# Kernel tuning notes

Hardware: AMD Instinct MI355X
Metric: run time of the kernel (lower is better)

The kernel has to match this reference:

```python
import jax, jax.numpy as jnp
import numpy as np

EPS_BN = 1e-5     # torch BatchNorm1d default eps
EPS_NORM = 1e-12  # torch F.normalize default eps


def _l2norm(x):
    n = jnp.linalg.norm(x, axis=-1, keepdims=True)
    return x / jnp.maximum(n, EPS_NORM)


def setup_inputs() -> dict:
    key = jax.random.key(0)
    ks = jax.random.split(key, 12)
    B, D, H, Z, E, C = 8192, 2048, 2048, 256, 5, 100

    def rn(k, shape, scale=1.0):
        return jax.random.normal(k, shape, dtype=jnp.float32) * scale

    feats = rn(ks[0], (B, D))
    # head_pattern: MLP(D->H->Z) with BN(H), prototypes Linear(Z->E, no bias)
    pW1 = rn(ks[1], (D, H), 1.0 / np.sqrt(D))
    pb1 = jnp.zeros((H,), jnp.float32)
    pg = jnp.ones((H,), jnp.float32)
    pbt = jnp.zeros((H,), jnp.float32)
    pm = jnp.zeros((H,), jnp.float32)
    pv = jnp.ones((H,), jnp.float32)
    pW2 = rn(ks[2], (H, Z), 1.0 / np.sqrt(H))
    pb2 = jnp.zeros((Z,), jnp.float32)
    pProto = _l2norm(rn(ks[3], (E, Z)))  # normalize_prototypes()
    # head_class: E experts, each MLP(Z->H->Z) with BN(H), prototypes Linear(Z->C, no bias)
    cW1 = rn(ks[4], (E, Z, H), 1.0 / np.sqrt(Z))
    cb1 = jnp.zeros((E, H), jnp.float32)
    cg = jnp.ones((E, H), jnp.float32)
    cbt = jnp.zeros((E, H), jnp.float32)
    cm = jnp.zeros((E, H), jnp.float32)
    cv = jnp.ones((E, H), jnp.float32)
    cW2 = rn(ks[5], (E, H, Z), 1.0 / np.sqrt(H))
    cb2 = jnp.zeros((E, Z), jnp.float32)
    cProto = _l2norm(rn(ks[6], (E, C, Z)))
    return dict(feats=feats, pW1=pW1, pb1=pb1, pg=pg, pbt=pbt, pm=pm, pv=pv,
                pW2=pW2, pb2=pb2, pProto=pProto, cW1=cW1, cb1=cb1, cg=cg,
                cbt=cbt, cm=cm, cv=cv, cW2=cW2, cb2=cb2, cProto=cProto)


def reference(feats, pW1, pb1, pg, pbt, pm, pv, pW2, pb2, pProto,
              cW1, cb1, cg, cbt, cm, cv, cW2, cb2, cProto):
    E = cW1.shape[0]
    # --- head_pattern (expert 0 only) ---
    h = feats @ pW1 + pb1                                   # [B,H]
    h = (h - pm) * jax.lax.rsqrt(pv + EPS_BN) * pg + pbt    # BN (eval)
    h = jax.nn.relu(h)
    zp = _l2norm(h @ pW2 + pb2)                             # proj_feats_pattern [B,Z]
    logits_pattern = zp @ pProto.T                          # [B,E]
    # --- routing: argmax over pattern logits ---
    route = jnp.argmax(logits_pattern, axis=1)              # [B]
    onehot = jax.nn.one_hot(route, E, dtype=zp.dtype)       # [B,E]
    # --- all experts densely, then per-sample select (E=5 is small) ---
    h2 = jnp.einsum('bz,ezh->ebh', zp, cW1) + cb1[:, None, :]          # [E,B,H]
    h2 = (h2 - cm[:, None, :]) * jax.lax.rsqrt(cv[:, None, :] + EPS_BN) \
         * cg[:, None, :] + cbt[:, None, :]
    h2 = jax.nn.relu(h2)
    z2 = _l2norm(jnp.einsum('ebh,ehz->ebz', h2, cW2) + cb2[:, None, :])  # [E,B,Z]
    lc = jnp.einsum('ebz,ecz->ebc', z2, cProto)                          # [E,B,C]
    logits_class = jnp.einsum('be,ebc->bc', onehot, lc)                  # [B,C]
    proj_feats_class = jnp.einsum('be,ebz->bz', onehot, z2)              # [B,Z]
    return logits_pattern, zp, logits_class, proj_feats_class
```

## Files before the change

kernel.cpp:

```cpp
#include <hip/hip_runtime.h>
#include <math.h>

#define EPS_BN   1e-5f
#define EPS_NORM 1e-12f
#define GAP_TAU  1e-3f
#define RMAX     1024

constexpr int B_ = 8192, D_ = 2048, H_ = 2048, Z_ = 256, E_ = 5, C_ = 100;

typedef __attribute__((ext_vector_type(8))) short short8v;
typedef __attribute__((ext_vector_type(4))) float f32x4;
typedef __attribute__((ext_vector_type(8))) unsigned short ush8;
typedef __attribute__((ext_vector_type(4))) unsigned short ush4;

#define MFMA16(a,b,c) __builtin_amdgcn_mfma_f32_16x16x32_bf16(a,b,c,0,0,0)

#define GLD_LDS16(SRC, DST) \
  __builtin_amdgcn_global_load_lds((const __attribute__((address_space(1))) void*)(SRC), \
                                   (__attribute__((address_space(3))) void*)(DST), 16, 0, 0)

__device__ inline unsigned short f2bf(float x) {
    union { float f; unsigned u; } a; a.f = x;
    unsigned r = a.u + 0x7FFFu + ((a.u >> 16) & 1u);
    return (unsigned short)(r >> 16);
}
__device__ inline float bf2f(unsigned short u) {
    union { float f; unsigned v; } a; a.v = ((unsigned)u) << 16;
    return a.f;
}

__global__ void zero_counts(int* counts) {
    if (threadIdx.x < 8) counts[threadIdx.x] = 0;
}

__global__ __launch_bounds__(256)
void pack_rows(const float* __restrict__ in, unsigned short* __restrict__ out, int K)
{
    const size_t base = ((size_t)blockIdx.x * 256 + threadIdx.x) * 8;
    const size_t row = base / (size_t)K;
    const int col = (int)(base % (size_t)K);
    const float4 v0 = *(const float4*)&in[base];
    const float4 v1 = *(const float4*)&in[base + 4];
    float v[8] = {v0.x, v0.y, v0.z, v0.w, v1.x, v1.y, v1.z, v1.w};
    ush8 hv, lv;
#pragma unroll
    for (int j = 0; j < 8; ++j) {
        unsigned short hi = f2bf(v[j]);
        hv[j] = hi;
        lv[j] = f2bf(v[j] - bf2f(hi));
    }
    const size_t ob = ((size_t)row * (K >> 5) + (col >> 5)) * 64 + (col & 31);
    *(ush8*)&out[ob] = hv;
    *(ush8*)&out[ob + 32] = lv;
}

template<bool PACKED>
__global__ __launch_bounds__(256)
void tconv_kernel(const float* __restrict__ in, unsigned short* __restrict__ out,
                  int K, int N)
{
    __shared__ float tile[32][33];
    const int kt = blockIdx.x, nt = blockIdx.y;
    const size_t inB = (size_t)blockIdx.z * K * N;
    const int t = threadIdx.x;
    const int lr = t >> 5, lc = t & 31;
#pragma unroll
    for (int i = 0; i < 4; ++i) {
        const int k = kt * 32 + lr + i * 8;
        tile[lr + i * 8][lc] = in[inB + (size_t)k * N + nt * 32 + lc];
    }
    __syncthreads();
    const int n_loc = t >> 3, s = t & 7;
    const int n = nt * 32 + n_loc;
    if (PACKED) {
        const size_t ob = (size_t)blockIdx.z * N * K * 2 +
                          ((size_t)n * (K >> 5) + kt) * 64;
        ush4 hv, lv;
#pragma unroll
        for (int j = 0; j < 4; ++j) {
            const float v = tile[s * 4 + j][n_loc];
            unsigned short hi = f2bf(v);
            hv[j] = hi;
            lv[j] = f2bf(v - bf2f(hi));
        }
        *(ush4*)&out[ob + s * 4] = hv;
        *(ush4*)&out[ob + 32 + s * 4] = lv;
    } else {
        const size_t ob = (size_t)blockIdx.z * N * K + (size_t)n * K + kt * 32;
        ush4 hv;
#pragma unroll
        for (int j = 0; j < 4; ++j) hv[j] = f2bf(tile[s * 4 + j][n_loc]);
        *(ush4*)&out[ob + s * 4] = hv;
    }
}

template<int BM, int BN, int EPI>
__global__ __launch_bounds__(256)
void gemm_split3(const unsigned short* __restrict__ Apk,
                 const unsigned short* __restrict__ Bpk,
                 const float* __restrict__ bias,
                 const float* __restrict__ g, const float* __restrict__ bt,
                 const float* __restrict__ mean, const float* __restrict__ var,
                 void* __restrict__ outp, int K, int N)
{
    constexpr int WM = BM / 2, WN = BN / 2, FM = WM / 16, FN = WN / 16;
    constexpr int ROWS = BM + BN, TI = ROWS / 8, PW = TI / 4;
    __shared__ __align__(16) unsigned short lds[ROWS * 64];
    const int tid = threadIdx.x, waveId = tid >> 6, lane = tid & 63;
    const int aRowBase = blockIdx.y * BM, bColBase = blockIdx.x * BN;
    const int wRow = (waveId >> 1) * WM, wCol = (waveId & 1) * WN;
    const int Kg = K >> 5;
    const int sr = lane >> 3, ss = lane & 7;

    f32x4 acc[FM][FN] = {};

    for (int kg = 0; kg < Kg; ++kg) {
#pragma unroll
        for (int t = 0; t < PW; ++t) {
            const int q = waveId * PW + t;
            const int r = q * 8 + sr;
            const int c = ss ^ (r & 7);
            const unsigned short* src;
            if (r < BM) src = Apk + ((size_t)(aRowBase + r) * Kg + kg) * 64 + c * 8;
            else        src = Bpk + ((size_t)(bColBase + (r - BM)) * Kg + kg) * 64 + c * 8;
            GLD_LDS16(src, &lds[q * 512]);
        }
        __syncthreads();
        short8v a_hi[FM], a_lo[FM], b_hi[FN], b_lo[FN];
#pragma unroll
        for (int fm = 0; fm < FM; ++fm) {
            const int r = wRow + fm * 16 + (lane & 15);
            const int ch = lane >> 4;
            a_hi[fm] = *(const short8v*)&lds[r * 64 + ((ch) ^ (r & 7)) * 8];
            a_lo[fm] = *(const short8v*)&lds[r * 64 + ((ch + 4) ^ (r & 7)) * 8];
        }
#pragma unroll
        for (int fn = 0; fn < FN; ++fn) {
            const int r = BM + wCol + fn * 16 + (lane & 15);
            const int ch = lane >> 4;
            b_hi[fn] = *(const short8v*)&lds[r * 64 + ((ch) ^ (r & 7)) * 8];
            b_lo[fn] = *(const short8v*)&lds[r * 64 + ((ch + 4) ^ (r & 7)) * 8];
        }
#pragma unroll
        for (int fm = 0; fm < FM; ++fm)
#pragma unroll
            for (int fn = 0; fn < FN; ++fn) {
                acc[fm][fn] = MFMA16(a_hi[fm], b_hi[fn], acc[fm][fn]);
                acc[fm][fn] = MFMA16(a_hi[fm], b_lo[fn], acc[fm][fn]);
                acc[fm][fn] = MFMA16(a_lo[fm], b_hi[fn], acc[fm][fn]);
            }
        __syncthreads();
    }

#pragma unroll
    for (int fn = 0; fn < FN; ++fn) {
        const int col = bColBase + wCol + fn * 16 + (lane & 15);
        const float bcol = bias[col];
        float scl = 0.f, sft = 0.f;
        if constexpr (EPI == 0) {
            scl = rsqrtf(var[col] + EPS_BN) * g[col];
            sft = bt[col] - mean[col] * scl;
        }
#pragma unroll
        for (int fm = 0; fm < FM; ++fm)
#pragma unroll
            for (int reg = 0; reg < 4; ++reg) {
                const int row = aRowBase + wRow + fm * 16 + (lane >> 4) * 4 + reg;
                float v = acc[fm][fn][reg] + bcol;
                if constexpr (EPI == 0) {
                    v = fmaxf(v * scl + sft, 0.f);
                    unsigned short hi = f2bf(v);
                    unsigned short lo = f2bf(v - bf2f(hi));
                    unsigned short* o = (unsigned short*)outp;
                    const size_t idx = ((size_t)row * (N >> 5) + (col >> 5)) * 64 + (col & 31);
                    o[idx] = hi; o[idx + 32] = lo;
                } else {
                    ((float*)outp)[(size_t)row * N + col] = v;
                }
            }
    }
}

template<int BM, int BN, int EPI>
__global__ __launch_bounds__(256)
void gemm_plain1(const unsigned short* __restrict__ Ab,
                 const unsigned short* __restrict__ Bt_,
                 const float* __restrict__ bias,
                 const float* __restrict__ g, const float* __restrict__ bt,
                 const float* __restrict__ mean, const float* __restrict__ var,
                 void* __restrict__ outp, const int* __restrict__ counts,
                 const int* __restrict__ offsets, int K, int N)
{
    constexpr int WM = BM / 2, WN = BN / 2, FM = WM / 16, FN = WN / 16;
    constexpr int ROWS = BM + BN, TI = ROWS / 8, PW = TI / 4;
    const int e = blockIdx.z;
    const int cnt = counts[e];
    const int aRowBase = blockIdx.y * BM;
    if (aRowBase >= cnt) return;
    const int obase = offsets[e];
    __shared__ __align__(16) unsigned short lds[ROWS * 64];
    const int tid = threadIdx.x, waveId = tid >> 6, lane = tid & 63;
    const int bColBase = blockIdx.x * BN;
    const int wRow = (waveId >> 1) * WM, wCol = (waveId & 1) * WN;
    const unsigned short* A = Ab + (size_t)obase * K;
    const unsigned short* Bp = Bt_ + (size_t)e * N * K;
    const int sr = lane >> 3, ss = lane & 7;

    f32x4 acc[FM][FN] = {};

    for (int k0 = 0; k0 < K; k0 += 64) {
#pragma unroll
        for (int t = 0; t < PW; ++t) {
            const int q = waveId * PW + t;
            const int r = q * 8 + sr;
            const int c = ss ^ (r & 7);
            const unsigned short* src;
            if (r < BM) src = A + (size_t)(aRowBase + r) * K + k0 + c * 8;
            else        src = Bp + (size_t)(bColBase + (r - BM)) * K + k0 + c * 8;
            GLD_LDS16(src, &lds[q * 512]);
        }
        __syncthreads();
#pragma unroll
        for (int ks = 0; ks < 2; ++ks) {
            short8v a[FM], b[FN];
#pragma unroll
            for (int fm = 0; fm < FM; ++fm) {
                const int r = wRow + fm * 16 + (lane & 15);
                const int c = (ks * 4 + (lane >> 4)) ^ (r & 7);
                a[fm] = *(const short8v*)&lds[r * 64 + c * 8];
            }
#pragma unroll
            for (int fn = 0; fn < FN; ++fn) {
                const int r = BM + wCol + fn * 16 + (lane & 15);
                const int c = (ks * 4 + (lane >> 4)) ^ (r & 7);
                b[fn] = *(const short8v*)&lds[r * 64 + c * 8];
            }
#pragma unroll
            for (int fm = 0; fm < FM; ++fm)
#pragma unroll
                for (int fn = 0; fn < FN; ++fn)
                    acc[fm][fn] = MFMA16(a[fm], b[fn], acc[fm][fn]);
        }
        __syncthreads();
    }

#pragma unroll
    for (int fn = 0; fn < FN; ++fn) {
        const int col = bColBase + wCol + fn * 16 + (lane & 15);
        const float bcol = bias[(size_t)e * N + col];
        float scl = 0.f, sft = 0.f;
        if constexpr (EPI == 2) {
            scl = rsqrtf(var[(size_t)e * N + col] + EPS_BN) * g[(size_t)e * N + col];
            sft = bt[(size_t)e * N + col] - mean[(size_t)e * N + col] * scl;
        }
#pragma unroll
        for (int fm = 0; fm < FM; ++fm)
#pragma unroll
            for (int reg = 0; reg < 4; ++reg) {
                const int gr = aRowBase + wRow + fm * 16 + (lane >> 4) * 4 + reg;
                if (gr < cnt) {
                    float v = acc[fm][fn][reg] + bcol;
                    if constexpr (EPI == 2) {
                        v = fmaxf(v * scl + sft, 0.f);
                        ((unsigned short*)outp)[(size_t)(obase + gr) * N + col] = f2bf(v);
                    } else {
                        ((float*)outp)[(size_t)(obase + gr) * N + col] = v;
                    }
                }
            }
    }
}

template<bool BN_RELU>
__global__ __launch_bounds__(256)
void gemm_kernel(const float* __restrict__ A, const float* __restrict__ W,
                 const float* __restrict__ bias,
                 const float* __restrict__ g, const float* __restrict__ bt,
                 const float* __restrict__ mean, const float* __restrict__ var,
                 float* __restrict__ Cout, int M, int N, int K)
{
    constexpr int BM = 64, BN = 64, BK = 16, TM = 4, TN = 4;
    __shared__ float As[BK][BM + 4];
    __shared__ float Ws[BK][BN + 4];
    const int tid = threadIdx.y * 16 + threadIdx.x;
    const int rowBase = blockIdx.y * BM;
    const int colBase = blockIdx.x * BN;
    const int aRow = tid >> 2, aCol = (tid & 3) * 4;
    const int wRow = tid >> 4, wCol = (tid & 15) * 4;
    float acc[TM][TN] = {};

    for (int k0 = 0; k0 < K; k0 += BK) {
        const float4 av = *reinterpret_cast<const float4*>(
            &A[(size_t)(rowBase + aRow) * K + k0 + aCol]);
        As[aCol + 0][aRow] = av.x; As[aCol + 1][aRow] = av.y;
        As[aCol + 2][aRow] = av.z; As[aCol + 3][aRow] = av.w;
        const float4 wv = *reinterpret_cast<const float4*>(
            &W[(size_t)(k0 + wRow) * N + colBase + wCol]);
        *reinterpret_cast<float4*>(&Ws[wRow][wCol]) = wv;
        __syncthreads();
#pragma unroll
        for (int kk = 0; kk < BK; ++kk) {
            float a[TM], w[TN];
#pragma unroll
            for (int i = 0; i < TM; ++i) a[i] = As[kk][threadIdx.y * TM + i];
#pragma unroll
            for (int j = 0; j < TN; ++j) w[j] = Ws[kk][threadIdx.x * TN + j];
#pragma unroll
            for (int i = 0; i < TM; ++i)
#pragma unroll
                for (int j = 0; j < TN; ++j)
                    acc[i][j] = fmaf(a[i], w[j], acc[i][j]);
        }
        __syncthreads();
    }
#pragma unroll
    for (int i = 0; i < TM; ++i) {
        const int row = rowBase + threadIdx.y * TM + i;
#pragma unroll
        for (int j = 0; j < TN; ++j) {
            const int col = colBase + threadIdx.x * TN + j;
            float v = acc[i][j] + bias[col];
            if constexpr (BN_RELU) {
                v = (v - mean[col]) * rsqrtf(var[col] + EPS_BN) * g[col] + bt[col];
                v = fmaxf(v, 0.f);
            }
            Cout[(size_t)row * N + col] = v;
        }
    }
}

__global__ __launch_bounds__(256)
void refine_gemm1(const float* __restrict__ feats, const float* __restrict__ W,
                  const float* __restrict__ bias, const float* __restrict__ g,
                  const float* __restrict__ bt, const float* __restrict__ mean,
                  const float* __restrict__ var,
                  const int* __restrict__ rlist, const int* __restrict__ counts,
                  float* __restrict__ outp)
{
    constexpr int BM = 64, BN = 64, BK = 16, TM = 4, TN = 4;
    const int cnt_raw = counts[5];
    const int cnt = cnt_raw > RMAX ? RMAX : cnt_raw;
    const int rowTile = blockIdx.y * BM;
    if (rowTile >= cnt) return;
    __shared__ float As[BK][BM + 4];
    __shared__ float Ws[BK][BN + 4];
    const int tid = threadIdx.y * 16 + threadIdx.x;
    const int colBase = blockIdx.x * BN;
    const int aRow = tid >> 2, aCol = (tid & 3) * 4;
    const int wRow = tid >> 4, wCol = (tid & 15) * 4;
    const int gi = rowTile + aRow;
    const int srcRow = (gi < cnt) ? rlist[gi] : 0;
    float acc[TM][TN] = {};

    for (int k0 = 0; k0 < D_; k0 += BK) {
        const float4 av = *reinterpret_cast<const float4*>(
            &feats[(size_t)srcRow * D_ + k0 + aCol]);
        As[aCol + 0][aRow] = av.x; As[aCol + 1][aRow] = av.y;
        As[aCol + 2][aRow] = av.z; As[aCol + 3][aRow] = av.w;
        const float4 wv = *reinterpret_cast<const float4*>(
            &W[(size_t)(k0 + wRow) * H_ + colBase + wCol]);
        *reinterpret_cast<float4*>(&Ws[wRow][wCol]) = wv;
        __syncthreads();
#pragma unroll
        for (int kk = 0; kk < BK; ++kk) {
            float a[TM], w[TN];
#pragma unroll
            for (int i = 0; i < TM; ++i) a[i] = As[kk][threadIdx.y * TM + i];
#pragma unroll
            for (int j = 0; j < TN; ++j) w[j] = Ws[kk][threadIdx.x * TN + j];
#pragma unroll
            for (int i = 0; i < TM; ++i)
#pragma unroll
                for (int j = 0; j < TN; ++j)
                    acc[i][j] = fmaf(a[i], w[j], acc[i][j]);
        }
        __syncthreads();
    }
#pragma unroll
    for (int i = 0; i < TM; ++i) {
        const int gr = rowTile + threadIdx.y * TM + i;
        if (gr >= cnt) continue;
#pragma unroll
        for (int j = 0; j < TN; ++j) {
            const int col = colBase + threadIdx.x * TN + j;
            float v = acc[i][j] + bias[col];
            v = (v - mean[col]) * rsqrtf(var[col] + EPS_BN) * g[col] + bt[col];
            outp[(size_t)gr * H_ + col] = fmaxf(v, 0.f);
        }
    }
}

__global__ __launch_bounds__(256)
void norm_rows(const float* __restrict__ in, float* __restrict__ ws_zp,
               float* __restrict__ out_zp)
{
    const int row = blockIdx.x, t = threadIdx.x;
    const float v = in[(size_t)row * Z_ + t];
    float s = v * v;
    for (int off = 32; off; off >>= 1) s += __shfl_down(s, off);
    __shared__ float wsum[4];
    if ((t & 63) == 0) wsum[t >> 6] = s;
    __syncthreads();
    const float tot = wsum[0] + wsum[1] + wsum[2] + wsum[3];
    const float scale = 1.f / fmaxf(sqrtf(tot), EPS_NORM);
    const float z = v * scale;
    ws_zp[(size_t)row * Z_ + t] = z;
    out_zp[(size_t)row * Z_ + t] = z;
}

__global__ __launch_bounds__(256)
void logits_flag(const float* __restrict__ zp, const float* __restrict__ pProto,
                 float* __restrict__ out_lp, int* __restrict__ counts,
                 int* __restrict__ rlist)
{
    const int wave = threadIdx.x >> 6, lane = threadIdx.x & 63;
    const int b = blockIdx.x * 4 + wave;
    const float4 z = *(const float4*)&zp[(size_t)b * Z_ + lane * 4];
    float p[E_];
#pragma unroll
    for (int e = 0; e < E_; ++e) {
        const float4 pr = *(const float4*)&pProto[(size_t)e * Z_ + lane * 4];
        float s = z.x * pr.x + z.y * pr.y + z.z * pr.z + z.w * pr.w;
        for (int off = 32; off; off >>= 1) s += __shfl_down(s, off);
        p[e] = s;
    }
    if (lane == 0) {
        float b1 = -1e30f, b2 = -1e30f;
#pragma unroll
        for (int e = 0; e < E_; ++e) {
            out_lp[(size_t)b * E_ + e] = p[e];
            if (p[e] > b1) { b2 = b1; b1 = p[e]; }
            else if (p[e] > b2) b2 = p[e];
        }
        if (b1 - b2 < GAP_TAU) {
            const int i = atomicAdd(&counts[5], 1);
            if (i < RMAX) rlist[i] = b;
        }
    }
}

__global__ __launch_bounds__(256)
void refine_finalize(const float* __restrict__ tR, const float* __restrict__ pProto,
                     const int* __restrict__ rlist, const int* __restrict__ counts,
                     float* __restrict__ out_lp)
{
    const int cnt_raw = counts[5];
    const int cnt = cnt_raw > RMAX ? RMAX : cnt_raw;
    const int i = blockIdx.x;
    if (i >= cnt) return;
    const int b = rlist[i];
    const int t = threadIdx.x;
    const float v = tR[(size_t)i * Z_ + t];
    __shared__ float wsum[4];
    float s = v * v;
    for (int off = 32; off; off >>= 1) s += __shfl_down(s, off);
    if ((t & 63) == 0) wsum[t >> 6] = s;
    __syncthreads();
    const float scale = 1.f / fmaxf(sqrtf(wsum[0] + wsum[1] + wsum[2] + wsum[3]), EPS_NORM);
    const float z = v * scale;
    for (int e = 0; e < E_; ++e) {
        float d = z * pProto[(size_t)e * Z_ + t];
        for (int off = 32; off; off >>= 1) d += __shfl_down(d, off);
        __syncthreads();
        if ((t & 63) == 0) wsum[t >> 6] = d;
        __syncthreads();
        if (t == 0) out_lp[(size_t)b * E_ + e] = wsum[0] + wsum[1] + wsum[2] + wsum[3];
    }
}

__global__ __launch_bounds__(256)
void route_kernel(const float* __restrict__ lp, int* __restrict__ counts,
                  int* __restrict__ lists)
{
    const int b = blockIdx.x * 256 + threadIdx.x;
    const float* p = lp + (size_t)b * E_;
    int best = 0; float bv = p[0];
#pragma unroll
    for (int e = 1; e < E_; ++e) { const float x = p[e]; if (x > bv) { bv = x; best = e; } }
    const int pos = atomicAdd(&counts[best], 1);
    lists[best * B_ + pos] = b;
}

__global__ void calc_offsets(const int* __restrict__ counts, int* __restrict__ offsets) {
    if (threadIdx.x == 0) {
        int acc = 0;
        for (int e = 0; e < E_; ++e) { offsets[e] = acc; acc += counts[e]; }
        offsets[E_] = acc;
    }
}

__global__ __launch_bounds__(64)
void gather_zpc(const float* __restrict__ zp, const int* __restrict__ lists,
                const int* __restrict__ offsets, unsigned short* __restrict__ zpc)
{
    const int c = blockIdx.x;
    int e = 0;
#pragma unroll
    for (int k = 1; k < E_; ++k) if (c >= offsets[k]) e = k;
    const int b = lists[e * B_ + (c - offsets[e])];
    const int t = threadIdx.x;
    const float4 v = *(const float4*)&zp[(size_t)b * Z_ + t * 4];
    ush4 o = { f2bf(v.x), f2bf(v.y), f2bf(v.z), f2bf(v.w) };
    *(ush4*)&zpc[(size_t)c * Z_ + t * 4] = o;
}

__global__ __launch_bounds__(256)
void finalize(const float* __restrict__ z2c, const float* __restrict__ cProto,
              const int* __restrict__ lists, const int* __restrict__ offsets,
              float* __restrict__ out_lc, float* __restrict__ out_pf)
{
    const int c = blockIdx.x;
    const int t = threadIdx.x;
    int e = 0;
#pragma unroll
    for (int k = 1; k < E_; ++k) if (c >= offsets[k]) e = k;
    const int b = lists[e * B_ + (c - offsets[e])];

    const float v = z2c[(size_t)c * Z_ + t];
    float s = v * v;
    for (int off = 32; off; off >>= 1) s += __shfl_down(s, off);
    __shared__ float wsum[4];
    if ((t & 63) == 0) wsum[t >> 6] = s;
    __syncthreads();
    const float tot = wsum[0] + wsum[1] + wsum[2] + wsum[3];
    const float scale = 1.f / fmaxf(sqrtf(tot), EPS_NORM);
    const float z = v * scale;
    out_pf[(size_t)b * Z_ + t] = z;

    __shared__ float zn[Z_];
    zn[t] = z;
    __syncthreads();
    if (t < C_) {
        const float* pr = &cProto[((size_t)e * C_ + t) * Z_];
        float acc = 0.f;
        for (int zi = 0; zi < Z_; ++zi) acc = fmaf(zn[zi], pr[zi], acc);
        out_lc[(size_t)b * C_ + t] = acc;
    }
}

extern "C" void kernel_launch(void* const* d_in, const int* in_sizes, int n_in,
                              void* d_out, int out_size, void* d_ws, size_t ws_size,
                              hipStream_t stream)
{
    const float* feats  = (const float*)d_in[0];
    const float* pW1    = (const float*)d_in[1];
    const float* pb1    = (const float*)d_in[2];
    const float* pg     = (const float*)d_in[3];
    const float* pbt    = (const float*)d_in[4];
    const float* pm     = (const float*)d_in[5];
    const float* pv     = (const float*)d_in[6];
    const float* pW2    = (const float*)d_in[7];
    const float* pb2    = (const float*)d_in[8];
    const float* pProto = (const float*)d_in[9];
    const float* cW1    = (const float*)d_in[10];
    const float* cb1    = (const float*)d_in[11];
    const float* cg     = (const float*)d_in[12];
    const float* cbt    = (const float*)d_in[13];
    const float* cm     = (const float*)d_in[14];
    const float* cv     = (const float*)d_in[15];
    const float* cW2    = (const float*)d_in[16];
    const float* cb2    = (const float*)d_in[17];
    const float* cProto = (const float*)d_in[18];

    unsigned short* fAp  = (unsigned short*)d_ws;
    unsigned short* hpk  = fAp  + (size_t)B_ * D_ * 2;
    unsigned short* W1Tp = hpk  + (size_t)B_ * H_ * 2;
    unsigned short* W2Tp = W1Tp + (size_t)H_ * D_ * 2;
    unsigned short* cW1T = W2Tp + (size_t)Z_ * H_ * 2;
    unsigned short* cW2T = cW1T + (size_t)E_ * H_ * Z_;
    unsigned short* zpc  = cW2T + (size_t)E_ * Z_ * H_;
    float* zp  = (float*)(zpc + (size_t)(B_ + 128) * Z_);
    float* z2c = zp + (size_t)B_ * Z_;
    int* counts  = (int*)(z2c + (size_t)(B_ + 128) * Z_);
    int* offsets = counts + 8;
    int* rlist   = offsets + 8;
    int* lists   = rlist + RMAX;
    unsigned short* h2c = fAp;
    float* hR = (float*)hpk;
    float* tR = hR + (size_t)RMAX * H_;

    float* out_lp = (float*)d_out;
    float* out_zp = out_lp + (size_t)B_ * E_;
    float* out_lc = out_zp + (size_t)B_ * Z_;
    float* out_pf = out_lc + (size_t)B_ * C_;

    zero_counts<<<1, 64, 0, stream>>>(counts);

    pack_rows<<<(int)(((size_t)B_ * D_) / 2048), 256, 0, stream>>>(feats, fAp, D_);
    tconv_kernel<true ><<<dim3(D_ / 32, H_ / 32, 1), 256, 0, stream>>>(pW1, W1Tp, D_, H_);
    tconv_kernel<true ><<<dim3(H_ / 32, Z_ / 32, 1), 256, 0, stream>>>(pW2, W2Tp, H_, Z_);
    tconv_kernel<false><<<dim3(Z_ / 32, H_ / 32, E_), 256, 0, stream>>>(cW1, cW1T, Z_, H_);
    tconv_kernel<false><<<dim3(H_ / 32, Z_ / 32, E_), 256, 0, stream>>>(cW2, cW2T, H_, Z_);

    gemm_split3<128, 128, 0><<<dim3(H_ / 128, B_ / 128), 256, 0, stream>>>(
        fAp, W1Tp, pb1, pg, pbt, pm, pv, hpk, D_, H_);
    gemm_split3<128, 64, 1><<<dim3(Z_ / 64, B_ / 128), 256, 0, stream>>>(
        hpk, W2Tp, pb2, nullptr, nullptr, nullptr, nullptr, zp, H_, Z_);

    norm_rows<<<B_, 256, 0, stream>>>(zp, zp, out_zp);
    logits_flag<<<B_ / 4, 256, 0, stream>>>(zp, pProto, out_lp, counts, rlist);

    refine_gemm1<<<dim3(H_ / 64, RMAX / 64), dim3(16, 16), 0, stream>>>(
        feats, pW1, pb1, pg, pbt, pm, pv, rlist, counts, hR);
    gemm_kernel<false><<<dim3(Z_ / 64, RMAX / 64), dim3(16, 16), 0, stream>>>(
        hR, pW2, pb2, nullptr, nullptr, nullptr, nullptr, tR, RMAX, Z_, H_);
    refine_finalize<<<RMAX, 256, 0, stream>>>(tR, pProto, rlist, counts, out_lp);

    route_kernel<<<B_ / 256, 256, 0, stream>>>(out_lp, counts, lists);
    calc_offsets<<<1, 64, 0, stream>>>(counts, offsets);
    gather_zpc<<<B_, 64, 0, stream>>>(zp, lists, offsets, zpc);

    gemm_plain1<128, 128, 2><<<dim3(H_ / 128, B_ / 128, E_), 256, 0, stream>>>(
        zpc, cW1T, cb1, cg, cbt, cm, cv, h2c, counts, offsets, Z_, H_);
    gemm_plain1<128, 128, 3><<<dim3(Z_ / 128, B_ / 128, E_), 256, 0, stream>>>(
        h2c, cW2T, cb2, nullptr, nullptr, nullptr, nullptr, z2c, counts, offsets, H_, Z_);

    finalize<<<B_, 256, 0, stream>>>(z2c, cProto, lists, offsets, out_lc, out_pf);
}
```

Before: 922.3 us.

## Fuse norm/logits, gather in GEMM, MFMA class logits, bound refine GEMM

Merges zero_counts into pack_rows and norm_rows into the logits kernel, which now also writes bf16 zp. The expert GEMM gathers rows directly through the routing lists, so the gather_zpc kernel is gone. Class logits move from a scalar per-row dot loop to a bf16 MFMA GEMM over a padded bf16 copy of cProto. The refine GEMM now exits early for tiles past the flagged-row count, and the split3 GEMMs precompute their load pointers outside the K loop. Doing the logits in bf16 lowers their precision, since only hi parts are used, with no split correction.

Measured after the change: 842.9 us. 8.6% less time.

```diff
diff --git a/kernel.cpp b/kernel.cpp
--- a/kernel.cpp
+++ b/kernel.cpp
@@ -29,13 +29,11 @@
     return a.f;
 }
 
-__global__ void zero_counts(int* counts) {
-    if (threadIdx.x < 8) counts[threadIdx.x] = 0;
-}
-
-__global__ __launch_bounds__(256)
-void pack_rows(const float* __restrict__ in, unsigned short* __restrict__ out, int K)
-{
+__global__ __launch_bounds__(256)
+void pack_rows(const float* __restrict__ in, unsigned short* __restrict__ out,
+               int K, int* __restrict__ counts)
+{
+    if (blockIdx.x == 0 && threadIdx.x < 8) counts[threadIdx.x] = 0;
     const size_t base = ((size_t)blockIdx.x * 256 + threadIdx.x) * 8;
     const size_t row = base / (size_t)K;
     const int col = (int)(base % (size_t)K);
@@ -92,6 +90,21 @@
         for (int j = 0; j < 4; ++j) hv[j] = f2bf(tile[s * 4 + j][n_loc]);
         *(ush4*)&out[ob + s * 4] = hv;
     }
+}
+
+__global__ __launch_bounds__(64)
+void conv_cproto(const float* __restrict__ cProto, unsigned short* __restrict__ out)
+{
+    const int e = blockIdx.x >> 7, r = blockIdx.x & 127;
+    const int t = threadIdx.x;
+    ush4 o;
+    if (r < C_) {
+        const float4 v = *(const float4*)&cProto[((size_t)e * C_ + r) * Z_ + t * 4];
+        o = ush4{ f2bf(v.x), f2bf(v.y), f2bf(v.z), f2bf(v.w) };
+    } else {
+        o = ush4{ 0, 0, 0, 0 };
+    }
+    *(ush4*)&out[((size_t)e * 128 + r) * Z_ + t * 4] = o;
 }
 
 template<int BM, int BN, int EPI>
@@ -112,18 +125,24 @@
     const int Kg = K >> 5;
     const int sr = lane >> 3, ss = lane & 7;
 
+    const unsigned short* sp[PW];
+#pragma unroll
+    for (int t = 0; t < PW; ++t) {
+        const int q = waveId * PW + t;
+        const int r = q * 8 + sr;
+        const int c = ss ^ (r & 7);
+        sp[t] = (r < BM)
+            ? Apk + ((size_t)(aRowBase + r) * Kg) * 64 + c * 8
+            : Bpk + ((size_t)(bColBase + (r - BM)) * Kg) * 64 + c * 8;
+    }
+
     f32x4 acc[FM][FN] = {};
 
     for (int kg = 0; kg < Kg; ++kg) {
 #pragma unroll
         for (int t = 0; t < PW; ++t) {
-            const int q = waveId * PW + t;
-            const int r = q * 8 + sr;
-            const int c = ss ^ (r & 7);
-            const unsigned short* src;
-            if (r < BM) src = Apk + ((size_t)(aRowBase + r) * Kg + kg) * 64 + c * 8;
-            else        src = Bpk + ((size_t)(bColBase + (r - BM)) * Kg + kg) * 64 + c * 8;
-            GLD_LDS16(src, &lds[q * 512]);
+            GLD_LDS16(sp[t], &lds[(waveId * PW + t) * 512]);
+            sp[t] += 64;
         }
         __syncthreads();
         short8v a_hi[FM], a_lo[FM], b_hi[FN], b_lo[FN];
@@ -181,7 +200,7 @@
     }
 }
 
-template<int BM, int BN, int EPI>
+template<int BM, int BN, int EPI, bool GATHER>
 __global__ __launch_bounds__(256)
 void gemm_plain1(const unsigned short* __restrict__ Ab,
                  const unsigned short* __restrict__ Bt_,
@@ -189,7 +208,8 @@
                  const float* __restrict__ g, const float* __restrict__ bt,
                  const float* __restrict__ mean, const float* __restrict__ var,
                  void* __restrict__ outp, const int* __restrict__ counts,
-                 const int* __restrict__ offsets, int K, int N)
+                 const int* __restrict__ offsets, const int* __restrict__ lists,
+                 int K, int N)
 {
     constexpr int WM = BM / 2, WN = BN / 2, FM = WM / 16, FN = WN / 16;
     constexpr int ROWS = BM + BN, TI = ROWS / 8, PW = TI / 4;
@@ -202,22 +222,35 @@
     const int tid = threadIdx.x, waveId = tid >> 6, lane = tid & 63;
     const int bColBase = blockIdx.x * BN;
     const int wRow = (waveId >> 1) * WM, wCol = (waveId & 1) * WN;
-    const unsigned short* A = Ab + (size_t)obase * K;
     const unsigned short* Bp = Bt_ + (size_t)e * N * K;
     const int sr = lane >> 3, ss = lane & 7;
 
+    const unsigned short* sp[PW];
+#pragma unroll
+    for (int t = 0; t < PW; ++t) {
+        const int q = waveId * PW + t;
+        const int r = q * 8 + sr;
+        const int c = ss ^ (r & 7);
+        if (r < BM) {
+            int gi = aRowBase + r;
+            if constexpr (GATHER) {
+                const int srcb = lists[e * B_ + (gi < cnt ? gi : cnt - 1)];
+                sp[t] = Ab + (size_t)srcb * K + c * 8;
+            } else {
+                sp[t] = Ab + (size_t)(obase + gi) * K + c * 8;
+            }
+        } else {
+            sp[t] = Bp + (size_t)(bColBase + (r - BM)) * K + c * 8;
+        }
+    }
+
     f32x4 acc[FM][FN] = {};
 
     for (int k0 = 0; k0 < K; k0 += 64) {
 #pragma unroll
         for (int t = 0; t < PW; ++t) {
-            const int q = waveId * PW + t;
-            const int r = q * 8 + sr;
-            const int c = ss ^ (r & 7);
-            const unsigned short* src;
-            if (r < BM) src = A + (size_t)(aRowBase + r) * K + k0 + c * 8;
-            else        src = Bp + (size_t)(bColBase + (r - BM)) * K + k0 + c * 8;
-            GLD_LDS16(src, &lds[q * 512]);
+            GLD_LDS16(sp[t], &lds[(waveId * PW + t) * 512]);
+            sp[t] += 64;
         }
         __syncthreads();
 #pragma unroll
@@ -271,61 +304,83 @@
     }
 }
 
-template<bool BN_RELU>
-__global__ __launch_bounds__(256)
-void gemm_kernel(const float* __restrict__ A, const float* __restrict__ W,
-                 const float* __restrict__ bias,
-                 const float* __restrict__ g, const float* __restrict__ bt,
-                 const float* __restrict__ mean, const float* __restrict__ var,
-                 float* __restrict__ Cout, int M, int N, int K)
-{
-    constexpr int BM = 64, BN = 64, BK = 16, TM = 4, TN = 4;
-    __shared__ float As[BK][BM + 4];
-    __shared__ float Ws[BK][BN + 4];
-    const int tid = threadIdx.y * 16 + threadIdx.x;
-    const int rowBase = blockIdx.y * BM;
-    const int colBase = blockIdx.x * BN;
-    const int aRow = tid >> 2, aCol = (tid & 3) * 4;
-    const int wRow = tid >> 4, wCol = (tid & 15) * 4;
-    float acc[TM][TN] = {};
-
-    for (int k0 = 0; k0 < K; k0 += BK) {
-        const float4 av = *reinterpret_cast<const float4*>(
-            &A[(size_t)(rowBase + aRow) * K + k0 + aCol]);
-        As[aCol + 0][aRow] = av.x; As[aCol + 1][aRow] = av.y;
-        As[aCol + 2][aRow] = av.z; As[aCol + 3][aRow] = av.w;
-        const float4 wv = *reinterpret_cast<const float4*>(
-            &W[(size_t)(k0 + wRow) * N + colBase + wCol]);
-        *reinterpret_cast<float4*>(&Ws[wRow][wCol]) = wv;
-        __syncthreads();
-#pragma unroll
-        for (int kk = 0; kk < BK; ++kk) {
-            float a[TM], w[TN];
-#pragma unroll
-            for (int i = 0; i < TM; ++i) a[i] = As[kk][threadIdx.y * TM + i];
-#pragma unroll
-            for (int j = 0; j < TN; ++j) w[j] = Ws[kk][threadIdx.x * TN + j];
-#pragma unroll
-            for (int i = 0; i < TM; ++i)
-#pragma unroll
-                for (int j = 0; j < TN; ++j)
-                    acc[i][j] = fmaf(a[i], w[j], acc[i][j]);
-        }
-        __syncthreads();
-    }
-#pragma unroll
-    for (int i = 0; i < TM; ++i) {
-        const int row = rowBase + threadIdx.y * TM + i;
-#pragma unroll
-        for (int j = 0; j < TN; ++j) {
-            const int col = colBase + threadIdx.x * TN + j;
-            float v = acc[i][j] + bias[col];
-            if constexpr (BN_RELU) {
-                v = (v - mean[col]) * rsqrtf(var[col] + EPS_BN) * g[col] + bt[col];
-                v = fmaxf(v, 0.f);
-            }
-            Cout[(size_t)row * N + col] = v;
-        }
+__global__ __launch_bounds__(256)
+void class_gemm(const unsigned short* __restrict__ Ab,
+                const unsigned short* __restrict__ Bt_,
+                const int* __restrict__ counts, const int* __restrict__ offsets,
+                const int* __restrict__ lists, float* __restrict__ out_lc)
+{
+    constexpr int BM = 128, BN = 128, FM = 4, FN = 4;
+    constexpr int ROWS = BM + BN, PW = (ROWS / 8) / 4;
+    constexpr int K = Z_;
+    const int e = blockIdx.z;
+    const int cnt = counts[e];
+    const int aRowBase = blockIdx.y * BM;
+    if (aRowBase >= cnt) return;
+    const int obase = offsets[e];
+    __shared__ __align__(16) unsigned short lds[ROWS * 64];
+    const int tid = threadIdx.x, waveId = tid >> 6, lane = tid & 63;
+    const int wRow = (waveId >> 1) * 64, wCol = (waveId & 1) * 64;
+    const unsigned short* Bp = Bt_ + (size_t)e * 128 * K;
+    const int sr = lane >> 3, ss = lane & 7;
+
+    const unsigned short* sp[PW];
+#pragma unroll
+    for (int t = 0; t < PW; ++t) {
+        const int q = waveId * PW + t;
+        const int r = q * 8 + sr;
+        const int c = ss ^ (r & 7);
+        sp[t] = (r < BM) ? Ab + (size_t)(obase + aRowBase + r) * K + c * 8
+                         : Bp + (size_t)(r - BM) * K + c * 8;
+    }
+
+    f32x4 acc[FM][FN] = {};
+
+    for (int k0 = 0; k0 < K; k0 += 64) {
+#pragma unroll
+        for (int t = 0; t < PW; ++t) {
+            GLD_LDS16(sp[t], &lds[(waveId * PW + t) * 512]);
+            sp[t] += 64;
+        }
+        __syncthreads();
+#pragma unroll
+        for (int ks = 0; ks < 2; ++ks) {
+            short8v a[FM], b[FN];
+#pragma unroll
+            for (int fm = 0; fm < FM; ++fm) {
+                const int r = wRow + fm * 16 + (lane & 15);
+                const int c = (ks * 4 + (lane >> 4)) ^ (r & 7);
+                a[fm] = *(const short8v*)&lds[r * 64 + c * 8];
+            }
+#pragma unroll
+            for (int fn = 0; fn < FN; ++fn) {
+                const int r = BM + wCol + fn * 16 + (lane & 15);
+                const int c = (ks * 4 + (lane >> 4)) ^ (r & 7);
+                b[fn] = *(const short8v*)&lds[r * 64 + c * 8];
+            }
+#pragma unroll
+            for (int fm = 0; fm < FM; ++fm)
+#pragma unroll
+                for (int fn = 0; fn < FN; ++fn)
+                    acc[fm][fn] = MFMA16(a[fm], b[fn], acc[fm][fn]);
+        }
+        __syncthreads();
+    }
+
+#pragma unroll
+    for (int fn = 0; fn < FN; ++fn) {
+        const int col = wCol + fn * 16 + (lane & 15);
+        if (col >= C_) continue;
+#pragma unroll
+        for (int fm = 0; fm < FM; ++fm)
+#pragma unroll
+            for (int reg = 0; reg < 4; ++reg) {
+                const int gr = aRowBase + wRow + fm * 16 + (lane >> 4) * 4 + reg;
+                if (gr < cnt) {
+                    const int b = lists[e * B_ + gr];
+                    out_lc[(size_t)b * C_ + col] = acc[fm][fn][reg];
+                }
+            }
     }
 }
 
@@ -391,38 +446,82 @@
 }
 
 __global__ __launch_bounds__(256)
-void norm_rows(const float* __restrict__ in, float* __restrict__ ws_zp,
-               float* __restrict__ out_zp)
-{
-    const int row = blockIdx.x, t = threadIdx.x;
-    const float v = in[(size_t)row * Z_ + t];
-    float s = v * v;
-    for (int off = 32; off; off >>= 1) s += __shfl_down(s, off);
-    __shared__ float wsum[4];
-    if ((t & 63) == 0) wsum[t >> 6] = s;
-    __syncthreads();
-    const float tot = wsum[0] + wsum[1] + wsum[2] + wsum[3];
-    const float scale = 1.f / fmaxf(sqrtf(tot), EPS_NORM);
-    const float z = v * scale;
-    ws_zp[(size_t)row * Z_ + t] = z;
-    out_zp[(size_t)row * Z_ + t] = z;
-}
-
-__global__ __launch_bounds__(256)
-void logits_flag(const float* __restrict__ zp, const float* __restrict__ pProto,
+void refine_gemm2(const float* __restrict__ A, const float* __restrict__ W,
+                  const float* __restrict__ bias, const int* __restrict__ counts,
+                  float* __restrict__ Cout)
+{
+    constexpr int BM = 64, BN = 64, BK = 16, TM = 4, TN = 4;
+    const int cnt_raw = counts[5];
+    const int cnt = cnt_raw > RMAX ? RMAX : cnt_raw;
+    const int rowTile = blockIdx.y * BM;
+    if (rowTile >= cnt) return;
+    __shared__ float As[BK][BM + 4];
+    __shared__ float Ws[BK][BN + 4];
+    const int tid = threadIdx.y * 16 + threadIdx.x;
+    const int colBase = blockIdx.x * BN;
+    const int aRow = tid >> 2, aCol = (tid & 3) * 4;
+    const int wRow = tid >> 4, wCol = (tid & 15) * 4;
+    float acc[TM][TN] = {};
+
+    for (int k0 = 0; k0 < H_; k0 += BK) {
+        const float4 av = *reinterpret_cast<const float4*>(
+            &A[(size_t)(rowTile + aRow) * H_ + k0 + aCol]);
+        As[aCol + 0][aRow] = av.x; As[aCol + 1][aRow] = av.y;
+        As[aCol + 2][aRow] = av.z; As[aCol + 3][aRow] = av.w;
+        const float4 wv = *reinterpret_cast<const float4*>(
+            &W[(size_t)(k0 + wRow) * Z_ + colBase + wCol]);
+        *reinterpret_cast<float4*>(&Ws[wRow][wCol]) = wv;
+        __syncthreads();
+#pragma unroll
+        for (int kk = 0; kk < BK; ++kk) {
+            float a[TM], w[TN];
+#pragma unroll
+            for (int i = 0; i < TM; ++i) a[i] = As[kk][threadIdx.y * TM + i];
+#pragma unroll
+            for (int j = 0; j < TN; ++j) w[j] = Ws[kk][threadIdx.x * TN + j];
+#pragma unroll
+            for (int i = 0; i < TM; ++i)
+#pragma unroll
+                for (int j = 0; j < TN; ++j)
+                    acc[i][j] = fmaf(a[i], w[j], acc[i][j]);
+        }
+        __syncthreads();
+    }
+#pragma unroll
+    for (int i = 0; i < TM; ++i) {
+        const int row = rowTile + threadIdx.y * TM + i;
+#pragma unroll
+        for (int j = 0; j < TN; ++j) {
+            const int col = colBase + threadIdx.x * TN + j;
+            Cout[(size_t)row * Z_ + col] = acc[i][j] + bias[col];
+        }
+    }
+}
+
+__global__ __launch_bounds__(256)
+void norm_logits(const float* __restrict__ zp, const float* __restrict__ pProto,
+                 float* __restrict__ out_zp, unsigned short* __restrict__ zpb,
                  float* __restrict__ out_lp, int* __restrict__ counts,
                  int* __restrict__ rlist)
 {
     const int wave = threadIdx.x >> 6, lane = threadIdx.x & 63;
     const int b = blockIdx.x * 4 + wave;
-    const float4 z = *(const float4*)&zp[(size_t)b * Z_ + lane * 4];
+    const float4 v = *(const float4*)&zp[(size_t)b * Z_ + lane * 4];
+    float s = v.x * v.x + v.y * v.y + v.z * v.z + v.w * v.w;
+    for (int off = 32; off; off >>= 1) s += __shfl_down(s, off);
+    s = __shfl(s, 0);
+    const float scale = 1.f / fmaxf(sqrtf(s), EPS_NORM);
+    float4 z = make_float4(v.x * scale, v.y * scale, v.z * scale, v.w * scale);
+    *(float4*)&out_zp[(size_t)b * Z_ + lane * 4] = z;
+    ush4 o = { f2bf(z.x), f2bf(z.y), f2bf(z.z), f2bf(z.w) };
+    *(ush4*)&zpb[(size_t)b * Z_ + lane * 4] = o;
     float p[E_];
 #pragma unroll
     for (int e = 0; e < E_; ++e) {
         const float4 pr = *(const float4*)&pProto[(size_t)e * Z_ + lane * 4];
-        float s = z.x * pr.x + z.y * pr.y + z.z * pr.z + z.w * pr.w;
-        for (int off = 32; off; off >>= 1) s += __shfl_down(s, off);
-        p[e] = s;
+        float d = z.x * pr.x + z.y * pr.y + z.z * pr.z + z.w * pr.w;
+        for (int off = 32; off; off >>= 1) d += __shfl_down(d, off);
+        p[e] = d;
     }
     if (lane == 0) {
         float b1 = -1e30f, b2 = -1e30f;
@@ -489,53 +588,26 @@
     }
 }
 
-__global__ __launch_bounds__(64)
-void gather_zpc(const float* __restrict__ zp, const int* __restrict__ lists,
-                const int* __restrict__ offsets, unsigned short* __restrict__ zpc)
-{
-    const int c = blockIdx.x;
+__global__ __launch_bounds__(256)
+void finalize_norm(const float* __restrict__ z2c, const int* __restrict__ lists,
+                   const int* __restrict__ offsets, float* __restrict__ out_pf,
+                   unsigned short* __restrict__ z2nb)
+{
+    const int wave = threadIdx.x >> 6, lane = threadIdx.x & 63;
+    const int c = blockIdx.x * 4 + wave;
     int e = 0;
 #pragma unroll
     for (int k = 1; k < E_; ++k) if (c >= offsets[k]) e = k;
     const int b = lists[e * B_ + (c - offsets[e])];
-    const int t = threadIdx.x;
-    const float4 v = *(const float4*)&zp[(size_t)b * Z_ + t * 4];
-    ush4 o = { f2bf(v.x), f2bf(v.y), f2bf(v.z), f2bf(v.w) };
-    *(ush4*)&zpc[(size_t)c * Z_ + t * 4] = o;
-}
-
-__global__ __launch_bounds__(256)
-void finalize(const float* __restrict__ z2c, const float* __restrict__ cProto,
-              const int* __restrict__ lists, const int* __restrict__ offsets,
-              float* __restrict__ out_lc, float* __restrict__ out_pf)
-{
-    const int c = blockIdx.x;
-    const int t = threadIdx.x;
-    int e = 0;
-#pragma unroll
-    for (int k = 1; k < E_; ++k) if (c >= offsets[k]) e = k;
-    const int b = lists[e * B_ + (c - offsets[e])];
-
-    const float v = z2c[(size_t)c * Z_ + t];
-    float s = v * v;
+    const float4 v = *(const float4*)&z2c[(size_t)c * Z_ + lane * 4];
+    float s = v.x * v.x + v.y * v.y + v.z * v.z + v.w * v.w;
     for (int off = 32; off; off >>= 1) s += __shfl_down(s, off);
-    __shared__ float wsum[4];
-    if ((t & 63) == 0) wsum[t >> 6] = s;
-    __syncthreads();
-    const float tot = wsum[0] + wsum[1] + wsum[2] + wsum[3];
-    const float scale = 1.f / fmaxf(sqrtf(tot), EPS_NORM);
-    const float z = v * scale;
-    out_pf[(size_t)b * Z_ + t] = z;
-
-    __shared__ float zn[Z_];
-    zn[t] = z;
-    __syncthreads();
-    if (t < C_) {
-        const float* pr = &cProto[((size_t)e * C_ + t) * Z_];
-        float acc = 0.f;
-        for (int zi = 0; zi < Z_; ++zi) acc = fmaf(zn[zi], pr[zi], acc);
-        out_lc[(size_t)b * C_ + t] = acc;
-    }
+    s = __shfl(s, 0);
+    const float scale = 1.f / fmaxf(sqrtf(s), EPS_NORM);
+    float4 z = make_float4(v.x * scale, v.y * scale, v.z * scale, v.w * scale);
+    *(float4*)&out_pf[(size_t)b * Z_ + lane * 4] = z;
+    ush4 o = { f2bf(z.x), f2bf(z.y), f2bf(z.z), f2bf(z.w) };
+    *(ush4*)&z2nb[(size_t)c * Z_ + lane * 4] = o;
 }
 
 extern "C" void kernel_launch(void* const* d_in, const int* in_sizes, int n_in,
@@ -568,14 +640,16 @@
     unsigned short* W2Tp = W1Tp + (size_t)H_ * D_ * 2;
     unsigned short* cW1T = W2Tp + (size_t)Z_ * H_ * 2;
     unsigned short* cW2T = cW1T + (size_t)E_ * H_ * Z_;
-    unsigned short* zpc  = cW2T + (size_t)E_ * Z_ * H_;
-    float* zp  = (float*)(zpc + (size_t)(B_ + 128) * Z_);
+    unsigned short* cPb  = cW2T + (size_t)E_ * Z_ * H_;
+    unsigned short* zpb  = cPb  + (size_t)E_ * 128 * Z_;
+    float* zp  = (float*)(zpb + (size_t)B_ * Z_);
     float* z2c = zp + (size_t)B_ * Z_;
-    int* counts  = (int*)(z2c + (size_t)(B_ + 128) * Z_);
+    int* counts  = (int*)(z2c + (size_t)B_ * Z_);
     int* offsets = counts + 8;
     int* rlist   = offsets + 8;
     int* lists   = rlist + RMAX;
-    unsigned short* h2c = fAp;
+    unsigned short* h2c  = fAp;
+    unsigned short* z2nb = zpb;
     float* hR = (float*)hpk;
     float* tR = hR + (size_t)RMAX * H_;
 
@@ -584,36 +658,35 @@
     float* out_lc = out_zp + (size_t)B_ * Z_;
     float* out_pf = out_lc + (size_t)B_ * C_;
 
-    zero_counts<<<1, 64, 0, stream>>>(counts);
-
-    pack_rows<<<(int)(((size_t)B_ * D_) / 2048), 256, 0, stream>>>(feats, fAp, D_);
+    pack_rows<<<(int)(((size_t)B_ * D_) / 2048), 256, 0, stream>>>(feats, fAp, D_, counts);
     tconv_kernel<true ><<<dim3(D_ / 32, H_ / 32, 1), 256, 0, stream>>>(pW1, W1Tp, D_, H_);
     tconv_kernel<true ><<<dim3(H_ / 32, Z_ / 32, 1), 256, 0, stream>>>(pW2, W2Tp, H_, Z_);
     tconv_kernel<false><<<dim3(Z_ / 32, H_ / 32, E_), 256, 0, stream>>>(cW1, cW1T, Z_, H_);
     tconv_kernel<false><<<dim3(H_ / 32, Z_ / 32, E_), 256, 0, stream>>>(cW2, cW2T, H_, Z_);
+    conv_cproto<<<E_ * 128, 64, 0, stream>>>(cProto, cPb);
 
     gemm_split3<128, 128, 0><<<dim3(H_ / 128, B_ / 128), 256, 0, stream>>>(
         fAp, W1Tp, pb1, pg, pbt, pm, pv, hpk, D_, H_);
     gemm_split3<128, 64, 1><<<dim3(Z_ / 64, B_ / 128), 256, 0, stream>>>(
         hpk, W2Tp, pb2, nullptr, nullptr, nullptr, nullptr, zp, H_, Z_);
 
-    norm_rows<<<B_, 256, 0, stream>>>(zp, zp, out_zp);
-    logits_flag<<<B_ / 4, 256, 0, stream>>>(zp, pProto, out_lp, counts, rlist);
+    norm_logits<<<B_ / 4, 256, 0, stream>>>(zp, pProto, out_zp, zpb, out_lp, counts, rlist);
 
     refine_gemm1<<<dim3(H_ / 64, RMAX / 64), dim3(16, 16), 0, stream>>>(
         feats, pW1, pb1, pg, pbt, pm, pv, rlist, counts, hR);
-    gemm_kernel<false><<<dim3(Z_ / 64, RMAX / 64), dim3(16, 16), 0, stream>>>(
-        hR, pW2, pb2, nullptr, nullptr, nullptr, nullptr, tR, RMAX, Z_, H_);
+    refine_gemm2<<<dim3(Z_ / 64, RMAX / 64), dim3(16, 16), 0, stream>>>(
+        hR, pW2, pb2, counts, tR);
     refine_finalize<<<RMAX, 256, 0, stream>>>(tR, pProto, rlist, counts, out_lp);
 
     route_kernel<<<B_ / 256, 256, 0, stream>>>(out_lp, counts, lists);
     calc_offsets<<<1, 64, 0, stream>>>(counts, offsets);
-    gather_zpc<<<B_, 64, 0, stream>>>(zp, lists, offsets, zpc);
-
-    gemm_plain1<128, 128, 2><<<dim3(H_ / 128, B_ / 128, E_), 256, 0, stream>>>(
-        zpc, cW1T, cb1, cg, cbt, cm, cv, h2c, counts, offsets, Z_, H_);
-    gemm_plain1<128, 128, 3><<<dim3(Z_ / 128, B_ / 128, E_), 256, 0, stream>>>(
-        h2c, cW2T, cb2, nullptr, nullptr, nullptr, nullptr, z2c, counts, offsets, H_, Z_);
-
-    finalize<<<B_, 256, 0, stream>>>(z2c, cProto, lists, offsets, out_lc, out_pf);
-}
+
+    gemm_plain1<128, 128, 2, true ><<<dim3(H_ / 128, B_ / 128, E_), 256, 0, stream>>>(
+        zpb, cW1T, cb1, cg, cbt, cm, cv, h2c, counts, offsets, lists, Z_, H_);
+    gemm_plain1<128, 128, 3, false><<<dim3(Z_ / 128, B_ / 128, E_), 256, 0, stream>>>(
+        h2c, cW2T, cb2, nullptr, nullptr, nullptr, nullptr, z2c, counts, offsets, nullptr, H_, Z_);
+
+    finalize_norm<<<B_ / 4, 256, 0, stream>>>(z2c, lists, offsets, out_pf, z2nb);
+    class_gemm<<<dim3(1, B_ / 128, E_), 256, 0, stream>>>(
+        z2nb, cPb, counts, offsets, lists, out_lc);
+}
```
